# Kernel optimization log

Measured on AMD Instinct MI355X. Metric: run time of the kernel, lower is better.

The kernel has to match this reference:

```python
import jax, jax.numpy as jnp
import numpy as np

N_USERS = 100000
N_MOVIES = 20000
N_EDGES = 600000
FEAT = 64
HID = 128
OUT = 64
N_TUPLES = 100000


def _sage(x_src, x_dst, src_idx, dst_idx, n_dst, Wl, bl, Wr):
    # PyG SAGEConv (mean aggr): lin_l(mean of gathered src feats) + lin_r(x_dst)
    msg = x_src[src_idx]                                        # [E, d_src]
    summ = jax.ops.segment_sum(msg, dst_idx, num_segments=n_dst)
    cnt = jax.ops.segment_sum(jnp.ones((src_idx.shape[0],), x_src.dtype),
                              dst_idx, num_segments=n_dst)
    mean = summ / jnp.maximum(cnt, 1.0)[:, None]
    return mean @ Wl.T + bl + x_dst @ Wr.T


def setup_inputs() -> dict:
    key = jax.random.key(0)
    ks = jax.random.split(key, 20)
    s = 0.05
    return {
        "movie_x": jax.random.normal(ks[0], (N_MOVIES, FEAT), jnp.float32),
        "user_idx": jax.random.randint(ks[1], (N_EDGES,), 0, N_USERS),
        "movie_idx": jax.random.randint(ks[2], (N_EDGES,), 0, N_MOVIES),
        "tuples_coo": jax.random.randint(ks[3], (2, N_TUPLES), 0, N_MOVIES),
        "user_emb": jax.random.normal(ks[4], (1, HID), jnp.float32) * s,
        "W1l": jax.random.normal(ks[5], (HID, FEAT), jnp.float32) * s,
        "b1": jnp.zeros((HID,), jnp.float32),
        "W1r": jax.random.normal(ks[6], (HID, HID), jnp.float32) * s,
        "W2l": jax.random.normal(ks[7], (HID, HID), jnp.float32) * s,
        "b2": jnp.zeros((HID,), jnp.float32),
        "W2r": jax.random.normal(ks[8], (HID, FEAT), jnp.float32) * s,
        "W3l": jax.random.normal(ks[9], (HID, HID), jnp.float32) * s,
        "b3": jnp.zeros((HID,), jnp.float32),
        "W3r": jax.random.normal(ks[10], (HID, HID), jnp.float32) * s,
        "Wlin1": jax.random.normal(ks[11], (OUT, HID), jnp.float32) * s,
        "blin1": jnp.zeros((OUT,), jnp.float32),
        "Wlin2": jax.random.normal(ks[12], (OUT, HID), jnp.float32) * s,
        "blin2": jnp.zeros((OUT,), jnp.float32),
    }


def reference(movie_x, user_idx, movie_idx, tuples_coo, user_emb,
              W1l, b1, W1r, W2l, b2, W2r, W3l, b3, W3r,
              Wlin1, blin1, Wlin2, blin2):
    n_users = N_USERS
    user_x0 = jnp.broadcast_to(user_emb, (n_users, HID))  # emb.weight.repeat
    # conv1: (movie -> user) rev_rates edges: src=movie_idx, dst=user_idx
    user_x = jax.nn.relu(_sage(movie_x, user_x0, movie_idx, user_idx, n_users, W1l, b1, W1r))
    # conv2: (user -> movie) rates edges: src=user_idx, dst=movie_idx
    movie_z = jax.nn.relu(_sage(user_x, movie_x, user_idx, movie_idx, N_MOVIES, W2l, b2, W2r))
    # conv3: (movie -> user) again
    user_z = jax.nn.relu(_sage(movie_z, user_x, movie_idx, user_idx, n_users, W3l, b3, W3r))
    z_user = user_z @ Wlin1.T + blin1
    z_movie = movie_z @ Wlin2.T + blin2
    X = jnp.vstack((z_user, z_movie))
    # relation_schema = ['user', 'movie']: offset movie indices by n_users
    new_index = jnp.vstack((tuples_coo[0], tuples_coo[1] + n_users))
    return X, new_index
```

## Files before the change

### kernel.cpp

```cpp
#include <hip/hip_runtime.h>

typedef __attribute__((ext_vector_type(8))) short short8;
typedef __attribute__((ext_vector_type(4))) float f32x4;

static const int NU = 100000;
static const int NM = 20000;
static const int NE = 600000;
static const int FEAT = 64;
static const int HID = 128;
static const int OUTD = 64;
static const int NTOT = NU + NM;
static const int NLIST = 2 * NE;
static const int CVT_TOT = 81920 + NM * FEAT;
static const int CVT_BLKS = (CVT_TOT + 255) / 256;
static const int IDX_BLKS = (100000 + 255) / 256;

static const int UB_SHIFT = 9;
static const int MB_SHIFT = 7;
static const int NBU = (NU + 511) >> 9;
static const int NBM = (NM + 127) >> 7;
static const int NBUCK = NBU + NBM;
static const int EPB = 4096;
static const int NPBLK = (NE + EPB - 1) / EPB;

__device__ inline float b2f(unsigned short h) {
    unsigned int u = ((unsigned int)h) << 16;
    float f; __builtin_memcpy(&f, &u, 4); return f;
}
__device__ inline unsigned short f2b(float f) {
    unsigned int u; __builtin_memcpy(&u, &f, 4);
    u += 0x7FFFu + ((u >> 16) & 1u);
    return (unsigned short)(u >> 16);
}
__device__ inline unsigned int pk2(float a, float b) {
    return (unsigned int)f2b(a) | ((unsigned int)f2b(b) << 16);
}
__device__ inline int wswz(int row, int bc, int rowbytes) {
    return row * rowbytes + (bc ^ ((row & 7) << 4));
}

__global__ __launch_bounds__(256) void k_hist_misc(
        const int* __restrict__ ui, const int* __restrict__ mi, int* __restrict__ ghist,
        const float* __restrict__ w1l, const float* __restrict__ w2l,
        const float* __restrict__ w2r, const float* __restrict__ w3l,
        const float* __restrict__ w3r, const float* __restrict__ wl1,
        const float* __restrict__ wl2, const float* __restrict__ mx,
        unsigned short* __restrict__ dst,
        const int* __restrict__ tpl, float* __restrict__ oidx,
        const float* __restrict__ ue, const float* __restrict__ w1r,
        const float* __restrict__ b1, float* __restrict__ c1) {
    __shared__ int h[NBUCK];
    const int b = blockIdx.x;
    const int tid = threadIdx.x;
    if (b < NPBLK) {
        for (int i = tid; i < NBUCK; i += 256) h[i] = 0;
        __syncthreads();
#pragma unroll
        for (int it = 0; it < EPB / 256; ++it) {
            int e = b * EPB + it * 256 + tid;
            if (e < NE) {
                atomicAdd(&h[ui[e] >> UB_SHIFT], 1);
                atomicAdd(&h[NBU + (mi[e] >> MB_SHIFT)], 1);
            }
        }
        __syncthreads();
        for (int i = tid; i < NBUCK; i += 256)
            if (h[i]) atomicAdd(&ghist[i], h[i]);
    } else if (b < NPBLK + CVT_BLKS) {
        int g = (b - NPBLK) * 256 + tid;
        if (g >= CVT_TOT) return;
        const float* s; int o;
        if      (g < 8192)   { s = w1l; o = g; }
        else if (g < 24576)  { s = w2l; o = g - 8192; }
        else if (g < 32768)  { s = w2r; o = g - 24576; }
        else if (g < 49152)  { s = w3l; o = g - 32768; }
        else if (g < 65536)  { s = w3r; o = g - 49152; }
        else if (g < 73728)  { s = wl1; o = g - 65536; }
        else if (g < 81920)  { s = wl2; o = g - 73728; }
        else                 { s = mx;  o = g - 81920; }
        dst[g] = f2b(s[o]);
    } else if (b < NPBLK + CVT_BLKS + IDX_BLKS) {
        int i = (b - NPBLK - CVT_BLKS) * 256 + tid;
        if (i < 100000) {
            oidx[i] = (float)tpl[i];
            oidx[100000 + i] = (float)(tpl[100000 + i] + NU);
        }
    } else {
        int hh = tid;
        if (hh < HID) {
            float a = 0.f;
#pragma unroll 16
            for (int k = 0; k < HID; ++k) a += ue[k] * w1r[hh * HID + k];
            c1[hh] = a + b1[hh];
        }
    }
}

__global__ __launch_bounds__(512) void k_bscan(const int* __restrict__ ghist,
                                               int* __restrict__ bb,
                                               int* __restrict__ gcur) {
    __shared__ int s[512];
    const int tid = threadIdx.x;
    int v = (tid < NBUCK) ? ghist[tid] : 0;
    s[tid] = v;
    __syncthreads();
#pragma unroll
    for (int off = 1; off < 512; off <<= 1) {
        int x = (tid >= off) ? s[tid - off] : 0;
        __syncthreads();
        s[tid] += x;
        __syncthreads();
    }
    int excl = s[tid] - v;
    if (tid < NBUCK) { bb[tid] = excl; gcur[tid] = excl; }
    if (tid == 511) bb[NBUCK] = s[511];
}

__global__ __launch_bounds__(256) void k_part(const int* __restrict__ ui,
                                              const int* __restrict__ mi,
                                              int* __restrict__ gcur,
                                              int* __restrict__ entries) {
    __shared__ int h[NBUCK], base[NBUCK], cur[NBUCK];
    const int tid = threadIdx.x;
    for (int i = tid; i < NBUCK; i += 256) h[i] = 0;
    __syncthreads();

    int eu[EPB / 256], em[EPB / 256];
#pragma unroll
    for (int it = 0; it < EPB / 256; ++it) {
        int e = blockIdx.x * EPB + it * 256 + tid;
        if (e < NE) {
            eu[it] = ui[e]; em[it] = mi[e];
            atomicAdd(&h[eu[it] >> UB_SHIFT], 1);
            atomicAdd(&h[NBU + (em[it] >> MB_SHIFT)], 1);
        } else eu[it] = -1;
    }
    __syncthreads();
    for (int i = tid; i < NBUCK; i += 256) {
        int c = h[i];
        base[i] = c ? atomicAdd(&gcur[i], c) : 0;
        cur[i] = 0;
    }
    __syncthreads();
#pragma unroll
    for (int it = 0; it < EPB / 256; ++it) {
        if (eu[it] < 0) continue;
        int u = eu[it], m = em[it];
        int bu = u >> UB_SHIFT;
        int o1 = base[bu] + atomicAdd(&cur[bu], 1);
        entries[o1] = (m << UB_SHIFT) | (u & 511);
        int bm = NBU + (m >> MB_SHIFT);
        int o2 = base[bm] + atomicAdd(&cur[bm], 1);
        entries[o2] = (u << MB_SHIFT) | (m & 127);
    }
}

__global__ __launch_bounds__(256) void k_csr(const int* __restrict__ bb,
                                             const int* __restrict__ entries,
                                             int* __restrict__ rp,
                                             int* __restrict__ list) {
    __shared__ int lcnt[512], lrp[512], lcur[512], ps[256];
    const int b = blockIdx.x;
    const int tid = threadIdx.x;
    const int s = bb[b], e = bb[b + 1];
    const bool isU = b < NBU;
    const int shift = isU ? UB_SHIFT : MB_SHIFT;
    const int mask = isU ? 511 : 127;
    const int n0 = isU ? (b << UB_SHIFT) : ((b - NBU) << MB_SHIFT);
    const int nNodes = isU ? min(512, NU - n0) : min(128, NM - n0);
    const int g0 = isU ? n0 : NU + n0;

    for (int i = tid; i < 512; i += 256) { lcnt[i] = 0; lcur[i] = 0; }
    __syncthreads();
    for (int i = s + tid; i < e; i += 256)
        atomicAdd(&lcnt[entries[i] & mask], 1);
    __syncthreads();
    int a0 = lcnt[2 * tid], a1 = lcnt[2 * tid + 1];
    int pr = a0 + a1;
    ps[tid] = pr;
    __syncthreads();
#pragma unroll
    for (int off = 1; off < 256; off <<= 1) {
        int x = (tid >= off) ? ps[tid - off] : 0;
        __syncthreads();
        ps[tid] += x;
        __syncthreads();
    }
    int excl = ps[tid] - pr;
    lrp[2 * tid] = excl;
    lrp[2 * tid + 1] = excl + a0;
    __syncthreads();
    for (int i = tid; i < nNodes; i += 256) rp[g0 + i] = s + lrp[i];
    if (b == NBUCK - 1 && tid == 0) rp[NTOT] = e;
    for (int i = s + tid; i < e; i += 256) {
        int p = entries[i];
        int dl = p & mask;
        int off = s + lrp[dl] + atomicAdd(&lcur[dl], 1);
        list[off] = p >> shift;
    }
}

template<int C>
__global__ __launch_bounds__(256) void k_gather_b(const unsigned short* __restrict__ src,
                                                  const int* __restrict__ rp,
                                                  const int* __restrict__ list,
                                                  unsigned short* __restrict__ dst,
                                                  int base, int n) {
    constexpr int TPN = C / 8;
    constexpr int NPB = 256 / TPN;
    const int node = blockIdx.x * NPB + threadIdx.x / TPN;
    if (node >= n) return;
    const int c8 = (threadIdx.x % TPN) * 8;
    const int g = base + node;
    const int s = rp[g], e = rp[g + 1];

    float a[8];
#pragma unroll
    for (int j = 0; j < 8; ++j) a[j] = 0.f;

    int i = s;
    for (; i + 1 < e; i += 2) {
        int r0 = list[i], r1 = list[i + 1];
        short8 v0 = *reinterpret_cast<const short8*>(src + (size_t)r0 * C + c8);
        short8 v1 = *reinterpret_cast<const short8*>(src + (size_t)r1 * C + c8);
#pragma unroll
        for (int j = 0; j < 8; ++j)
            a[j] += b2f((unsigned short)v0[j]) + b2f((unsigned short)v1[j]);
    }
    if (i < e) {
        int r0 = list[i];
        short8 v0 = *reinterpret_cast<const short8*>(src + (size_t)r0 * C + c8);
#pragma unroll
        for (int j = 0; j < 8; ++j) a[j] += b2f((unsigned short)v0[j]);
    }
    const float sc = 1.0f / (float)max(e - s, 1);
    short8 o;
#pragma unroll
    for (int j = 0; j < 8; ++j) o[j] = (short)f2b(a[j] * sc);
    *reinterpret_cast<short8*>(dst + (size_t)node * C + c8) = o;
}

template<int K, int NO, bool AVEC, bool RELU, bool F32OUT>
__global__ __launch_bounds__(256) void k_mf2(const unsigned short* __restrict__ X,
                                             const unsigned short* __restrict__ W,
                                             const float* __restrict__ vec,
                                             void* __restrict__ Yv, int M) {
    constexpr int KT = K / 32;
    constexpr int CG = NO / 16;
    constexpr int WB = NO * K * 2;
    constexpr int RB = K * 2;
    __shared__ __align__(16) char lds[WB];
    const int tid = threadIdx.x;
    const int lane = tid & 63;
    const int wv = tid >> 6;
    const int rbase = blockIdx.x * 128 + wv * 32;
    const int lr = lane & 15;
    const int kg = lane >> 4;

#pragma unroll
    for (int i = 0; i < WB / 16 / 256; ++i) {
        int idx = tid + i * 256;
        int row = idx / (RB / 16);
        int bc = (idx % (RB / 16)) * 16;
        *reinterpret_cast<uint4*>(lds + wswz(row, bc, RB)) =
            *reinterpret_cast<const uint4*>((const char*)W + idx * 16);
    }

    short8 xb[2][KT];
#pragma unroll
    for (int t = 0; t < 2; ++t) {
        int row = min(rbase + t * 16 + lr, M - 1);
#pragma unroll
        for (int kt = 0; kt < KT; ++kt)
            xb[t][kt] = *reinterpret_cast<const short8*>(
                X + (size_t)row * K + kt * 32 + kg * 8);
    }
    __syncthreads();

    f32x4 acc[2][CG];
#pragma unroll
    for (int t = 0; t < 2; ++t)
#pragma unroll
        for (int c = 0; c < CG; ++c) acc[t][c] = (f32x4){0.f, 0.f, 0.f, 0.f};

#pragma unroll
    for (int cg = 0; cg < CG; ++cg) {
        short8 wf[KT];
#pragma unroll
        for (int kt = 0; kt < KT; ++kt)
            wf[kt] = *reinterpret_cast<const short8*>(
                lds + wswz(cg * 16 + lr, kt * 64 + kg * 16, RB));
#pragma unroll
        for (int kt = 0; kt < KT; ++kt)
#pragma unroll
            for (int t = 0; t < 2; ++t)
                acc[t][cg] = __builtin_amdgcn_mfma_f32_16x16x32_bf16(
                    wf[kt], xb[t][kt], acc[t][cg], 0, 0, 0);
    }

#pragma unroll
    for (int t = 0; t < 2; ++t) {
        const int u = rbase + t * 16 + lr;
        if (u >= M) continue;
#pragma unroll
        for (int cg = 0; cg < CG; ++cg) {
            const int h0 = cg * 16 + kg * 4;
            float v[4];
#pragma unroll
            for (int r = 0; r < 4; ++r) v[r] = acc[t][cg][r];
            if (AVEC) {
                float4 vv = *reinterpret_cast<const float4*>(vec + h0);
                v[0] += vv.x; v[1] += vv.y; v[2] += vv.z; v[3] += vv.w;
            }
            if (RELU)
#pragma unroll
                for (int r = 0; r < 4; ++r) v[r] = fmaxf(v[r], 0.f);
            if (F32OUT) {
                float4 o = make_float4(v[0], v[1], v[2], v[3]);
                *reinterpret_cast<float4*>((float*)Yv + (size_t)u * NO + h0) = o;
            } else {
                uint2 o = make_uint2(pk2(v[0], v[1]), pk2(v[2], v[3]));
                *reinterpret_cast<uint2*>((unsigned short*)Yv + (size_t)u * NO + h0) = o;
            }
        }
    }
}

__global__ __launch_bounds__(256) void k_fused_u(
        const unsigned short* __restrict__ S3, const unsigned short* __restrict__ user_x,
        const unsigned short* __restrict__ W3r, const float* __restrict__ b3,
        const unsigned short* __restrict__ Wl1, const float* __restrict__ bl1,
        float* __restrict__ out, int M) {
    __shared__ __align__(16) char lds[49152];
    const int tid = threadIdx.x;
    const int lane = tid & 63;
    const int wv = tid >> 6;
    const int rbase = blockIdx.x * 128 + wv * 32;
    const int lr = lane & 15;
    const int kg = lane >> 4;

#pragma unroll
    for (int i = 0; i < 8; ++i) {
        int idx = tid + i * 256;
        int row = idx >> 4, bc = (idx & 15) << 4;
        *reinterpret_cast<uint4*>(lds + wswz(row, bc, 256)) =
            *reinterpret_cast<const uint4*>((const char*)W3r + idx * 16);
    }
#pragma unroll
    for (int i = 0; i < 4; ++i) {
        int idx = tid + i * 256;
        int row = idx >> 4, bc = (idx & 15) << 4;
        *reinterpret_cast<uint4*>(lds + 32768 + wswz(row, bc, 256)) =
            *reinterpret_cast<const uint4*>((const char*)Wl1 + idx * 16);
    }

    short8 xc[2][4];
#pragma unroll
    for (int t = 0; t < 2; ++t) {
        int row = min(rbase + t * 16 + lr, M - 1);
#pragma unroll
        for (int kt = 0; kt < 4; ++kt)
            xc[t][kt] = *reinterpret_cast<const short8*>(
                user_x + (size_t)row * HID + kt * 32 + kg * 8);
    }
    __syncthreads();

    f32x4 acc[2][8];
#pragma unroll
    for (int t = 0; t < 2; ++t)
#pragma unroll
        for (int c = 0; c < 8; ++c) acc[t][c] = (f32x4){0.f, 0.f, 0.f, 0.f};

#pragma unroll
    for (int cg = 0; cg < 8; ++cg) {
        short8 wr[4];
#pragma unroll
        for (int kt = 0; kt < 4; ++kt)
            wr[kt] = *reinterpret_cast<const short8*>(
                lds + wswz(cg * 16 + lr, kt * 64 + kg * 16, 256));
#pragma unroll
        for (int kt = 0; kt < 4; ++kt)
#pragma unroll
            for (int t = 0; t < 2; ++t)
                acc[t][cg] = __builtin_amdgcn_mfma_f32_16x16x32_bf16(
                    wr[kt], xc[t][kt], acc[t][cg], 0, 0, 0);
    }
    __syncthreads();

#pragma unroll
    for (int t = 0; t < 2; ++t) {
        const int ul = wv * 32 + t * 16 + lr;
        const int u = min(rbase + t * 16 + lr, M - 1);
#pragma unroll
        for (int cg = 0; cg < 8; ++cg) {
            const int h0 = cg * 16 + kg * 4;
            uint2 s3 = *reinterpret_cast<const uint2*>(S3 + (size_t)u * HID + h0);
            float4 vv = *reinterpret_cast<const float4*>(b3 + h0);
            float v0 = fmaxf(acc[t][cg][0] + b2f((unsigned short)(s3.x & 0xffff)) + vv.x, 0.f);
            float v1 = fmaxf(acc[t][cg][1] + b2f((unsigned short)(s3.x >> 16)) + vv.y, 0.f);
            float v2 = fmaxf(acc[t][cg][2] + b2f((unsigned short)(s3.y & 0xffff)) + vv.z, 0.f);
            float v3 = fmaxf(acc[t][cg][3] + b2f((unsigned short)(s3.y >> 16)) + vv.w, 0.f);
            uint2 pk = make_uint2(pk2(v0, v1), pk2(v2, v3));
            *reinterpret_cast<uint2*>(lds + wswz(ul, h0 * 2, 256)) = pk;
        }
    }
    __syncthreads();

    short8 zb[2][4];
#pragma unroll
    for (int t = 0; t < 2; ++t) {
        const int ul = wv * 32 + t * 16 + lr;
#pragma unroll
        for (int kt = 0; kt < 4; ++kt)
            zb[t][kt] = *reinterpret_cast<const short8*>(
                lds + wswz(ul, kt * 64 + kg * 16, 256));
    }
    f32x4 a2[2][4];
#pragma unroll
    for (int t = 0; t < 2; ++t)
#pragma unroll
        for (int c = 0; c < 4; ++c) a2[t][c] = (f32x4){0.f, 0.f, 0.f, 0.f};
#pragma unroll
    for (int cg = 0; cg < 4; ++cg) {
        short8 wf[4];
#pragma unroll
        for (int kt = 0; kt < 4; ++kt)
            wf[kt] = *reinterpret_cast<const short8*>(
                lds + 32768 + wswz(cg * 16 + lr, kt * 64 + kg * 16, 256));
#pragma unroll
        for (int kt = 0; kt < 4; ++kt)
#pragma unroll
            for (int t = 0; t < 2; ++t)
                a2[t][cg] = __builtin_amdgcn_mfma_f32_16x16x32_bf16(
                    wf[kt], zb[t][kt], a2[t][cg], 0, 0, 0);
    }
#pragma unroll
    for (int t = 0; t < 2; ++t) {
        const int u = rbase + t * 16 + lr;
        if (u >= M) continue;
#pragma unroll
        for (int cg = 0; cg < 4; ++cg) {
            const int o0 = cg * 16 + kg * 4;
            float4 bb = *reinterpret_cast<const float4*>(bl1 + o0);
            float4 o = make_float4(a2[t][cg][0] + bb.x, a2[t][cg][1] + bb.y,
                                   a2[t][cg][2] + bb.z, a2[t][cg][3] + bb.w);
            *reinterpret_cast<float4*>(out + (size_t)u * OUTD + o0) = o;
        }
    }
}

__global__ __launch_bounds__(256) void k_fused_m(
        const unsigned short* __restrict__ mean2, const unsigned short* __restrict__ mxb,
        const unsigned short* __restrict__ W2l, const unsigned short* __restrict__ W2r,
        const float* __restrict__ b2, unsigned short* __restrict__ movie_z,
        const unsigned short* __restrict__ Wl2, const float* __restrict__ bl2,
        const unsigned short* __restrict__ W3l, unsigned short* __restrict__ Y3,
        float* __restrict__ out, int M) {
    __shared__ __align__(16) char lds[65536];
    const int tid = threadIdx.x;
    const int lane = tid & 63;
    const int wv = tid >> 6;
    const int rbase = blockIdx.x * 128 + wv * 32;
    const int lr = lane & 15;
    const int kg = lane >> 4;

#pragma unroll
    for (int i = 0; i < 8; ++i) {
        int idx = tid + i * 256;
        int row = idx >> 4, bc = (idx & 15) << 4;
        *reinterpret_cast<uint4*>(lds + wswz(row, bc, 256)) =
            *reinterpret_cast<const uint4*>((const char*)W2l + idx * 16);
    }
#pragma unroll
    for (int i = 0; i < 4; ++i) {
        int idx = tid + i * 256;
        int row = idx >> 3, bc = (idx & 7) << 4;
        *reinterpret_cast<uint4*>(lds + 32768 + wswz(row, bc, 128)) =
            *reinterpret_cast<const uint4*>((const char*)W2r + idx * 16);
        int row2 = idx >> 4, bc2 = (idx & 15) << 4;
        *reinterpret_cast<uint4*>(lds + 49152 + wswz(row2, bc2, 256)) =
            *reinterpret_cast<const uint4*>((const char*)Wl2 + idx * 16);
    }

    short8 xa[2][4], xc[2][2];
#pragma unroll
    for (int t = 0; t < 2; ++t) {
        int row = min(rbase + t * 16 + lr, M - 1);
#pragma unroll
        for (int kt = 0; kt < 4; ++kt)
            xa[t][kt] = *reinterpret_cast<const short8*>(
                mean2 + (size_t)row * HID + kt * 32 + kg * 8);
#pragma unroll
        for (int kt = 0; kt < 2; ++kt)
            xc[t][kt] = *reinterpret_cast<const short8*>(
                mxb + (size_t)row * FEAT + kt * 32 + kg * 8);
    }
    __syncthreads();

    f32x4 acc[2][8];
#pragma unroll
    for (int t = 0; t < 2; ++t)
#pragma unroll
        for (int c = 0; c < 8; ++c) acc[t][c] = (f32x4){0.f, 0.f, 0.f, 0.f};

#pragma unroll
    for (int cg = 0; cg < 8; ++cg) {
        short8 wl[4], wr[2];
#pragma unroll
        for (int kt = 0; kt < 4; ++kt)
            wl[kt] = *reinterpret_cast<const short8*>(
                lds + wswz(cg * 16 + lr, kt * 64 + kg * 16, 256));
#pragma unroll
        for (int kt = 0; kt < 2; ++kt)
            wr[kt] = *reinterpret_cast<const short8*>(
                lds + 32768 + wswz(cg * 16 + lr, kt * 64 + kg * 16, 128));
#pragma unroll
        for (int kt = 0; kt < 4; ++kt)
#pragma unroll
            for (int t = 0; t < 2; ++t)
                acc[t][cg] = __builtin_amdgcn_mfma_f32_16x16x32_bf16(
                    wl[kt], xa[t][kt], acc[t][cg], 0, 0, 0);
#pragma unroll
        for (int kt = 0; kt < 2; ++kt)
#pragma unroll
            for (int t = 0; t < 2; ++t)
                acc[t][cg] = __builtin_amdgcn_mfma_f32_16x16x32_bf16(
                    wr[kt], xc[t][kt], acc[t][cg], 0, 0, 0);
    }
    __syncthreads();

#pragma unroll
    for (int t = 0; t < 2; ++t) {
        const int ul = wv * 32 + t * 16 + lr;
        const int u = rbase + t * 16 + lr;
#pragma unroll
        for (int cg = 0; cg < 8; ++cg) {
            const int h0 = cg * 16 + kg * 4;
            float4 vv = *reinterpret_cast<const float4*>(b2 + h0);
            float v0 = fmaxf(acc[t][cg][0] + vv.x, 0.f);
            float v1 = fmaxf(acc[t][cg][1] + vv.y, 0.f);
            float v2 = fmaxf(acc[t][cg][2] + vv.z, 0.f);
            float v3 = fmaxf(acc[t][cg][3] + vv.w, 0.f);
            uint2 pk = make_uint2(pk2(v0, v1), pk2(v2, v3));
            *reinterpret_cast<uint2*>(lds + wswz(ul, h0 * 2, 256)) = pk;
            if (u < M)
                *reinterpret_cast<uint2*>(movie_z + (size_t)u * HID + h0) = pk;
        }
    }
    __syncthreads();

    short8 zb[2][4];
#pragma unroll
    for (int t = 0; t < 2; ++t) {
        const int ul = wv * 32 + t * 16 + lr;
#pragma unroll
        for (int kt = 0; kt < 4; ++kt)
            zb[t][kt] = *reinterpret_cast<const short8*>(
                lds + wswz(ul, kt * 64 + kg * 16, 256));
    }
    f32x4 a2[2][4];
#pragma unroll
    for (int t = 0; t < 2; ++t)
#pragma unroll
        for (int c = 0; c < 4; ++c) a2[t][c] = (f32x4){0.f, 0.f, 0.f, 0.f};
#pragma unroll
    for (int cg = 0; cg < 4; ++cg) {
        short8 wf[4];
#pragma unroll
        for (int kt = 0; kt < 4; ++kt)
            wf[kt] = *reinterpret_cast<const short8*>(
                lds + 49152 + wswz(cg * 16 + lr, kt * 64 + kg * 16, 256));
#pragma unroll
        for (int kt = 0; kt < 4; ++kt)
#pragma unroll
            for (int t = 0; t < 2; ++t)
                a2[t][cg] = __builtin_amdgcn_mfma_f32_16x16x32_bf16(
                    wf[kt], zb[t][kt], a2[t][cg], 0, 0, 0);
    }
#pragma unroll
    for (int t = 0; t < 2; ++t) {
        const int u = rbase + t * 16 + lr;
        if (u >= M) continue;
#pragma unroll
        for (int cg = 0; cg < 4; ++cg) {
            const int o0 = cg * 16 + kg * 4;
            float4 bb = *reinterpret_cast<const float4*>(bl2 + o0);
            float4 o = make_float4(a2[t][cg][0] + bb.x, a2[t][cg][1] + bb.y,
                                   a2[t][cg][2] + bb.z, a2[t][cg][3] + bb.w);
            *reinterpret_cast<float4*>(out + (size_t)u * OUTD + o0) = o;
        }
    }
    __syncthreads();

#pragma unroll
    for (int i = 0; i < 8; ++i) {
        int idx = tid + i * 256;
        int row = idx >> 4, bc = (idx & 15) << 4;
        *reinterpret_cast<uint4*>(lds + 32768 + wswz(row, bc, 256)) =
            *reinterpret_cast<const uint4*>((const char*)W3l + idx * 16);
    }
    __syncthreads();

    f32x4 a3[2][8];
#pragma unroll
    for (int t = 0; t < 2; ++t)
#pragma unroll
        for (int c = 0; c < 8; ++c) a3[t][c] = (f32x4){0.f, 0.f, 0.f, 0.f};
#pragma unroll
    for (int cg = 0; cg < 8; ++cg) {
        short8 wf[4];
#pragma unroll
        for (int kt = 0; kt < 4; ++kt)
            wf[kt] = *reinterpret_cast<const short8*>(
                lds + 32768 + wswz(cg * 16 + lr, kt * 64 + kg * 16, 256));
#pragma unroll
        for (int kt = 0; kt < 4; ++kt)
#pragma unroll
            for (int t = 0; t < 2; ++t)
                a3[t][cg] = __builtin_amdgcn_mfma_f32_16x16x32_bf16(
                    wf[kt], zb[t][kt], a3[t][cg], 0, 0, 0);
    }
#pragma unroll
    for (int t = 0; t < 2; ++t) {
        const int u = rbase + t * 16 + lr;
        if (u >= M) continue;
#pragma unroll
        for (int cg = 0; cg < 8; ++cg) {
            const int h0 = cg * 16 + kg * 4;
            uint2 pk = make_uint2(pk2(a3[t][cg][0], a3[t][cg][1]),
                                  pk2(a3[t][cg][2], a3[t][cg][3]));
            *reinterpret_cast<uint2*>(Y3 + (size_t)u * HID + h0) = pk;
        }
    }
}

extern "C" void kernel_launch(void* const* d_in, const int* in_sizes, int n_in,
                              void* d_out, int out_size, void* d_ws, size_t ws_size,
                              hipStream_t stream) {
    const float* movie_x  = (const float*)d_in[0];
    const int*   user_idx = (const int*)d_in[1];
    const int*   movie_idx= (const int*)d_in[2];
    const int*   tuples   = (const int*)d_in[3];
    const float* user_emb = (const float*)d_in[4];
    const float* W1l = (const float*)d_in[5];
    const float* b1  = (const float*)d_in[6];
    const float* W1r = (const float*)d_in[7];
    const float* W2l = (const float*)d_in[8];
    const float* b2  = (const float*)d_in[9];
    const float* W2r = (const float*)d_in[10];
    const float* W3l = (const float*)d_in[11];
    const float* b3  = (const float*)d_in[12];
    const float* W3r = (const float*)d_in[13];
    const float* Wlin1 = (const float*)d_in[14];
    const float* blin1 = (const float*)d_in[15];
    const float* Wlin2 = (const float*)d_in[16];
    const float* blin2 = (const float*)d_in[17];

    float* out = (float*)d_out;

    char* p = (char*)d_ws;
    int* ghist = (int*)p;  p += 360 * 4;
    int* bb    = (int*)p;  p += 360 * 4;
    int* gcur  = (int*)p;  p += 360 * 4;
    int* entries = (int*)p; p += (size_t)NLIST * 4;
    int* rp    = (int*)p;  p += (size_t)(NTOT + 8) * 4;
    int* list  = (int*)p;  p += (size_t)NLIST * 4;
    float* c1  = (float*)p; p += 128 * 4;
    unsigned short* wb = (unsigned short*)p; p += (size_t)CVT_TOT * 2;
    unsigned short* W1l_b  = wb;
    unsigned short* W2l_b  = wb + 8192;
    unsigned short* W2r_b  = wb + 24576;
    unsigned short* W3l_b  = wb + 32768;
    unsigned short* W3r_b  = wb + 49152;
    unsigned short* Wlin1_b= wb + 65536;
    unsigned short* Wlin2_b= wb + 73728;
    unsigned short* mxb    = wb + 81920;
    unsigned short* mean1  = (unsigned short*)p; p += (size_t)NU * FEAT * 2;
    unsigned short* user_x = (unsigned short*)p; p += (size_t)NU * HID * 2;
    unsigned short* mean2  = (unsigned short*)p; p += (size_t)NM * HID * 2;
    unsigned short* movie_z= (unsigned short*)p; p += (size_t)NM * HID * 2;
    unsigned short* Y3     = (unsigned short*)p; p += (size_t)NM * HID * 2;
    unsigned short* S3     = (unsigned short*)p; p += (size_t)NU * HID * 2;

    hipMemsetAsync(ghist, 0, NBUCK * sizeof(int), stream);
    k_hist_misc<<<NPBLK + CVT_BLKS + IDX_BLKS + 1, 256, 0, stream>>>(
        user_idx, movie_idx, ghist,
        W1l, W2l, W2r, W3l, W3r, Wlin1, Wlin2, movie_x, wb,
        tuples, out + (size_t)(NU + NM) * OUTD, user_emb, W1r, b1, c1);
    k_bscan<<<1, 512, 0, stream>>>(ghist, bb, gcur);
    k_part<<<NPBLK, 256, 0, stream>>>(user_idx, movie_idx, gcur, entries);
    k_csr<<<NBUCK, 256, 0, stream>>>(bb, entries, rp, list);

    k_gather_b<FEAT><<<(NU + 31) / 32, 256, 0, stream>>>(mxb, rp, list, mean1, 0, NU);
    k_mf2<FEAT, HID, true, true, false><<<(NU + 127) / 128, 256, 0, stream>>>(
        mean1, W1l_b, c1, user_x, NU);

    k_gather_b<HID><<<(NM + 15) / 16, 256, 0, stream>>>(user_x, rp, list, mean2, NU, NM);
    k_fused_m<<<(NM + 127) / 128, 256, 0, stream>>>(
        mean2, mxb, W2l_b, W2r_b, b2, movie_z, Wlin2_b, blin2, W3l_b, Y3,
        out + (size_t)NU * OUTD, NM);

    k_gather_b<HID><<<(NU + 15) / 16, 256, 0, stream>>>(Y3, rp, list, S3, 0, NU);
    k_fused_u<<<(NU + 127) / 128, 256, 0, stream>>>(
        S3, user_x, W3r_b, b3, Wlin1_b, blin1, out, NU);
}
```

Baseline: 167.2 us.

## Project movie features before aggregation in conv1, fuse mean+bias+ReLU into gather

Reorders conv1 so the 64->128 linear projection is applied to the 20k movie rows first, then the projected rows are mean-aggregated per user with bias and ReLU fused into the gather. This replaces a 100k-row GEMM with a 20k-row GEMM and removes the mean1 intermediate, at the cost of gathering 128-wide instead of 64-wide rows for 600k edges. The projection GEMM is launched before the CSR build, so it can run independently of it.

```diff
diff --git a/kernel.cpp b/kernel.cpp
--- a/kernel.cpp
+++ b/kernel.cpp
@@ -240,6 +240,50 @@
     *reinterpret_cast<short8*>(dst + (size_t)node * C + c8) = o;
 }
 
+__global__ __launch_bounds__(256) void k_gather_relu(const unsigned short* __restrict__ Y1,
+                                                     const int* __restrict__ rp,
+                                                     const int* __restrict__ list,
+                                                     const float* __restrict__ c1,
+                                                     unsigned short* __restrict__ user_x,
+                                                     int n) {
+    const int node = blockIdx.x * 16 + threadIdx.x / 16;
+    if (node >= n) return;
+    const int c8 = (threadIdx.x % 16) * 8;
+    const int s = rp[node], e = rp[node + 1];
+
+    float a[8];
+#pragma unroll
+    for (int j = 0; j < 8; ++j) a[j] = 0.f;
+
+    int i = s;
+    for (; i + 1 < e; i += 2) {
+        int r0 = list[i], r1 = list[i + 1];
+        short8 v0 = *reinterpret_cast<const short8*>(Y1 + (size_t)r0 * HID + c8);
+        short8 v1 = *reinterpret_cast<const short8*>(Y1 + (size_t)r1 * HID + c8);
+#pragma unroll
+        for (int j = 0; j < 8; ++j)
+            a[j] += b2f((unsigned short)v0[j]) + b2f((unsigned short)v1[j]);
+    }
+    if (i < e) {
+        int r0 = list[i];
+        short8 v0 = *reinterpret_cast<const short8*>(Y1 + (size_t)r0 * HID + c8);
+#pragma unroll
+        for (int j = 0; j < 8; ++j) a[j] += b2f((unsigned short)v0[j]);
+    }
+    const float sc = 1.0f / (float)max(e - s, 1);
+    float4 cv0 = *reinterpret_cast<const float4*>(c1 + c8);
+    float4 cv1 = *reinterpret_cast<const float4*>(c1 + c8 + 4);
+    float r[8];
+    r[0] = fmaxf(a[0] * sc + cv0.x, 0.f); r[1] = fmaxf(a[1] * sc + cv0.y, 0.f);
+    r[2] = fmaxf(a[2] * sc + cv0.z, 0.f); r[3] = fmaxf(a[3] * sc + cv0.w, 0.f);
+    r[4] = fmaxf(a[4] * sc + cv1.x, 0.f); r[5] = fmaxf(a[5] * sc + cv1.y, 0.f);
+    r[6] = fmaxf(a[6] * sc + cv1.z, 0.f); r[7] = fmaxf(a[7] * sc + cv1.w, 0.f);
+    uint4 o;
+    o.x = pk2(r[0], r[1]); o.y = pk2(r[2], r[3]);
+    o.z = pk2(r[4], r[5]); o.w = pk2(r[6], r[7]);
+    *reinterpret_cast<uint4*>(user_x + (size_t)node * HID + c8) = o;
+}
+
 template<int K, int NO, bool AVEC, bool RELU, bool F32OUT>
 __global__ __launch_bounds__(256) void k_mf2(const unsigned short* __restrict__ X,
                                              const unsigned short* __restrict__ W,
@@ -675,7 +719,7 @@
     unsigned short* Wlin1_b= wb + 65536;
     unsigned short* Wlin2_b= wb + 73728;
     unsigned short* mxb    = wb + 81920;
-    unsigned short* mean1  = (unsigned short*)p; p += (size_t)NU * FEAT * 2;
+    unsigned short* Y1     = (unsigned short*)p; p += (size_t)NM * HID * 2;
     unsigned short* user_x = (unsigned short*)p; p += (size_t)NU * HID * 2;
     unsigned short* mean2  = (unsigned short*)p; p += (size_t)NM * HID * 2;
     unsigned short* movie_z= (unsigned short*)p; p += (size_t)NM * HID * 2;
@@ -687,13 +731,13 @@
         user_idx, movie_idx, ghist,
         W1l, W2l, W2r, W3l, W3r, Wlin1, Wlin2, movie_x, wb,
         tuples, out + (size_t)(NU + NM) * OUTD, user_emb, W1r, b1, c1);
+    k_mf2<FEAT, HID, false, false, false><<<(NM + 127) / 128, 256, 0, stream>>>(
+        mxb, W1l_b, nullptr, Y1, NM);
     k_bscan<<<1, 512, 0, stream>>>(ghist, bb, gcur);
     k_part<<<NPBLK, 256, 0, stream>>>(user_idx, movie_idx, gcur, entries);
     k_csr<<<NBUCK, 256, 0, stream>>>(bb, entries, rp, list);
 
-    k_gather_b<FEAT><<<(NU + 31) / 32, 256, 0, stream>>>(mxb, rp, list, mean1, 0, NU);
-    k_mf2<FEAT, HID, true, true, false><<<(NU + 127) / 128, 256, 0, stream>>>(
-        mean1, W1l_b, c1, user_x, NU);
+    k_gather_relu<<<(NU + 15) / 16, 256, 0, stream>>>(Y1, rp, list, c1, user_x, NU);
 
     k_gather_b<HID><<<(NM + 15) / 16, 256, 0, stream>>>(user_x, rp, list, mean2, NU, NM);
     k_fused_m<<<(NM + 127) / 128, 256, 0, stream>>>(
```

New measurement: 166.8 us. About the same (-0.3%).
